# Kernel optimization log

Measured on AMD Instinct MI355X. Metric: run time of the kernel, lower is better.

Reference implementation:

```python
import jax, jax.numpy as jnp
import numpy as np

B, S, D_MODEL, D_ATT = 4, 4096, 512, 64
EPS = 1e-5


def setup_inputs() -> dict:
    key = jax.random.key(0)
    ks = jax.random.split(key, 10)
    s_in = 1.0 / np.sqrt(D_MODEL)
    return {
        "x": jax.random.normal(ks[0], (B, S, D_MODEL), jnp.float32),
        "Wq": jax.random.uniform(ks[1], (D_MODEL, D_ATT), jnp.float32, -s_in, s_in),
        "bq": jax.random.uniform(ks[2], (D_ATT,), jnp.float32, -s_in, s_in),
        "Wk": jax.random.uniform(ks[3], (D_MODEL, D_ATT), jnp.float32, -s_in, s_in),
        "bk": jax.random.uniform(ks[4], (D_ATT,), jnp.float32, -s_in, s_in),
        "Wv": jax.random.uniform(ks[5], (D_MODEL, D_MODEL), jnp.float32, -s_in, s_in),
        "bv": jax.random.uniform(ks[6], (D_MODEL,), jnp.float32, -s_in, s_in),
        "gamma": jnp.ones((D_MODEL,), jnp.float32),
        "beta": jnp.zeros((D_MODEL,), jnp.float32),
    }


def reference(x, Wq, bq, Wk, bk, Wv, bv, gamma, beta):
    # Linear projections (torch Linear: x @ W^T + b; here W stored as [in, out])
    q = jnp.einsum("bsd,de->bse", x, Wq) + bq          # [B,S,d_att]
    k = jnp.einsum("bsd,de->bse", x, Wk) + bk          # [B,S,d_att]
    v = jnp.einsum("bsd,de->bse", x, Wv) + bv          # [B,S,d_model]
    # NOTE: original has NO 1/sqrt(d) scaling -- faithful to source.
    scores = jnp.einsum("bqe,bke->bqk", q, k)          # [B,S,S]
    seq = x.shape[1]
    causal = jnp.tril(jnp.ones((seq, seq), dtype=bool))
    scores = jnp.where(causal, scores, -jnp.inf)
    attn = jax.nn.softmax(scores, axis=-1)
    o = jnp.einsum("bqk,bkd->bqd", attn, v)            # [B,S,d_model]
    # residual + LayerNorm over last dim
    y = x + o
    mu = jnp.mean(y, axis=-1, keepdims=True)
    var = jnp.mean(jnp.square(y - mu), axis=-1, keepdims=True)
    return (y - mu) * jax.lax.rsqrt(var + EPS) * gamma + beta
```

## Files before the change

kernel.cpp:

```cpp
#include <hip/hip_runtime.h>

#define NB 4
#define SEQ 4096
#define DM 512
#define DA 64
#define LOG2E 1.44269504f

typedef __attribute__((ext_vector_type(8))) short bf16x8;
typedef __attribute__((ext_vector_type(4))) float f32x4;
typedef __attribute__((ext_vector_type(16))) float f32x16;
typedef __attribute__((address_space(3))) unsigned int lds_u32;
typedef const __attribute__((address_space(1))) unsigned int glb_u32;

__device__ __forceinline__ unsigned short f2bf(float f) {
  unsigned u = __float_as_uint(f);
  u += 0x7fffu + ((u >> 16) & 1u);
  return (unsigned short)(u >> 16);
}

__device__ __forceinline__ float bf2f(unsigned short h) {
  return __uint_as_float(((unsigned)h) << 16);
}

__device__ __forceinline__ unsigned cvt_pk_bf16(float lo, float hi) {
  unsigned r;
  asm("v_cvt_pk_bf16_f32 %0, %1, %2" : "=v"(r) : "v"(lo), "v"(hi));
  return r;
}

__device__ __forceinline__ float fexp2(float x) {
  float r;
  asm("v_exp_f32 %0, %1" : "=v"(r) : "v"(x));
  return r;
}

__device__ __forceinline__ void g2lds16(const unsigned short* g, unsigned short* l) {
  __builtin_amdgcn_global_load_lds((glb_u32*)g, (lds_u32*)l, 16, 0, 0);
}

__global__ void cast_x_kernel(const float* __restrict__ x, unsigned short* __restrict__ xb) {
  size_t i = ((size_t)blockIdx.x * blockDim.x + threadIdx.x) * 4;
  float4 v = *(const float4*)(x + i);
  ushort4 o;
  o.x = f2bf(v.x); o.y = f2bf(v.y); o.z = f2bf(v.z); o.w = f2bf(v.w);
  *(ushort4*)(xb + i) = o;
}

__global__ void prep_w_kernel(const float* __restrict__ Wq, const float* __restrict__ bq,
                              const float* __restrict__ Wk, const float* __restrict__ bk,
                              const float* __restrict__ Wv, const float* __restrict__ bv,
                              unsigned short* __restrict__ Wt, float* __restrict__ bias) {
  int n = blockIdx.x;
  for (int k = threadIdx.x; k < DM; k += blockDim.x) {
    float w;
    if (n < 64)       w = Wq[(size_t)k * DA + n];
    else if (n < 128) w = Wk[(size_t)k * DA + (n - 64)];
    else              w = Wv[(size_t)k * DM + (n - 128)];
    Wt[(size_t)n * DM + k] = f2bf(w);
  }
  if (threadIdx.x == 0)
    bias[n] = (n < 64) ? bq[n] : (n < 128) ? bk[n - 64] : bv[n - 128];
}

__launch_bounds__(256)
__global__ void proj_kernel(const unsigned short* __restrict__ xb,
                            const unsigned short* __restrict__ Wt,
                            const float* __restrict__ bias,
                            unsigned short* __restrict__ qws,
                            unsigned short* __restrict__ kp,
                            unsigned short* __restrict__ vp) {
  int C0 = blockIdx.x * 128;
  int R0 = blockIdx.y * 128;
  int tid = threadIdx.x;
  int w = tid >> 6, lane = tid & 63;
  int g = (lane >> 4) & 3, c15 = lane & 15;
  int wr = w >> 1, wc = w & 1;

  __shared__ unsigned short Ab[2][8192];
  __shared__ unsigned short Bb[2][8192];

  int row0 = tid >> 3;
  int scol = (tid & 7) ^ (row0 & 7);
  const unsigned short* srcA = xb + (size_t)(R0 + row0) * DM + scol * 8;
  const unsigned short* srcB = Wt + (size_t)(C0 + row0) * DM + scol * 8;

  auto stage = [&](int t, int kk) {
    for (int r = 0; r < 4; r++)
      g2lds16(srcA + (size_t)(r * 32) * DM + kk, &Ab[t][(r * 32 + w * 8) * 64]);
    for (int r = 0; r < 4; r++)
      g2lds16(srcB + (size_t)(r * 32) * DM + kk, &Bb[t][(r * 32 + w * 8) * 64]);
  };

  f32x4 acc[4][4];
#pragma unroll
  for (int i = 0; i < 4; i++)
#pragma unroll
    for (int j = 0; j < 4; j++) acc[i][j] = (f32x4)0.0f;

  stage(0, 0);
  __syncthreads();
  int t = 0;
  for (int s = 0; s < 8; s++) {
    if (s < 7) stage(t ^ 1, (s + 1) * 64);
    const unsigned short* A = &Ab[t][0];
    const unsigned short* B = &Bb[t][0];
#pragma unroll
    for (int kc = 0; kc < 2; kc++) {
      bf16x8 a[4], bb2[4];
#pragma unroll
      for (int i = 0; i < 4; i++) {
        int row = wr * 64 + i * 16 + c15;
        a[i] = *(const bf16x8*)&A[row * 64 + (((kc << 2) | g) ^ (row & 7)) * 8];
      }
#pragma unroll
      for (int j = 0; j < 4; j++) {
        int row = wc * 64 + j * 16 + c15;
        bb2[j] = *(const bf16x8*)&B[row * 64 + (((kc << 2) | g) ^ (row & 7)) * 8];
      }
#pragma unroll
      for (int i = 0; i < 4; i++)
#pragma unroll
        for (int j = 0; j < 4; j++)
          acc[i][j] = __builtin_amdgcn_mfma_f32_16x16x32_bf16(a[i], bb2[j], acc[i][j], 0, 0, 0);
    }
    __syncthreads();
    t ^= 1;
  }

  unsigned short* tw = (w < 2) ? (&Ab[0][0] + w * 4608) : (&Bb[0][0] + (w - 2) * 4608);
  int n0 = C0 + wc * 64;
#pragma unroll
  for (int j = 0; j < 4; j++) {
    int ncol = n0 + j * 16 + c15;
    float bv_ = bias[ncol];
    float qs = (ncol < 64) ? LOG2E : 1.0f;
#pragma unroll
    for (int i = 0; i < 4; i++)
#pragma unroll
      for (int r = 0; r < 4; r++) {
        int sl = i * 16 + g * 4 + r;
        tw[sl * 72 + j * 16 + c15] = f2bf((acc[i][j][r] + bv_) * qs);
      }
  }

  int RR = R0 + wr * 64;
  int b = RR >> 12, ktc = (RR & (SEQ - 1)) >> 6;
  if (n0 == 0) {
    for (int it = 0; it < 8; it++) {
      int rid = it * 64 + lane;
      int sl = rid >> 3, grp = rid & 7;
      bf16x8 vd = *(const bf16x8*)&tw[sl * 72 + grp * 8];
      *(bf16x8*)(qws + (size_t)(RR + sl) * DA + grp * 8) = vd;
    }
  } else if (n0 == 64) {
    for (int slot = 0; slot < 8; slot++) {
      bf16x8 vd = *(const bf16x8*)&tw[lane * 72 + slot * 8];
      *(bf16x8*)(kp + ((((size_t)b * 64 + ktc) * 8 + slot) * 64 + lane) * 8) = vd;
    }
  } else {
    int dvbase = n0 - 128;
    int dv = dvbase + lane;
    int dvc2 = dv >> 7, dvrow = dv & 127;
    for (int slot = 0; slot < 8; slot++) {
      union { unsigned short u[8]; bf16x8 h8; } pk;
#pragma unroll
      for (int j = 0; j < 8; j++) {
        int key = ((slot >> 2) << 5) | (((slot >> 1) & 1) << 4) | ((j >> 2) << 3) |
                  ((slot & 1) << 2) | (j & 3);
        pk.u[j] = tw[key * 72 + lane];
      }
      *(bf16x8*)(vp + (((((size_t)(b * 4 + dvc2)) * 64 + ktc) * 8 + slot) * 128 + dvrow) * 8) = pk.h8;
    }
  }
}

__launch_bounds__(256, 3)
__global__ void attn_kernel(const unsigned short* __restrict__ qws,
                            const unsigned short* __restrict__ kp,
                            const unsigned short* __restrict__ vp,
                            unsigned short* __restrict__ ob16) {
  int x = blockIdx.x, b = x >> 2, dvc = x & 3;
  int strip = 127 - blockIdx.y;
  int qrow32 = strip * 32;
  int n = (strip >> 1) + 1;
  int tid = threadIdx.x, w = tid >> 6, lane = tid & 63;
  int l31 = lane & 31, lh = lane >> 5;

  __shared__ unsigned short abuf[4][32][138];
  __shared__ float lbuf[4][32], Lfin[32];

  size_t bS = (size_t)b * SEQ;

  bf16x8 qf[4];
#pragma unroll
  for (int c = 0; c < 4; c++)
    qf[c] = *(const bf16x8*)(qws + (bS + qrow32 + l31) * DA + c * 16 + lh * 8);

  const unsigned short* kbase = kp + (size_t)b * 64 * 4096 + lh * 512 + l31 * 8;
  const unsigned short* vbase = vp + (size_t)(b * 4 + dvc) * 64 * 8192 + lh * 1024 + l31 * 8;

  f32x16 acc[4];
#pragma unroll
  for (int dt = 0; dt < 4; dt++) acc[dt] = (f32x16)0.0f;
  float la0 = 0.0f, la1 = 0.0f, la2 = 0.0f, la3 = 0.0f;

  for (int t = w; t < n; t += 4) {
    const unsigned short* kt_ = kbase + (size_t)t * 4096;
    const unsigned short* vt_ = vbase + (size_t)t * 8192;

    bf16x8 kf[4][2];
#pragma unroll
    for (int c = 0; c < 4; c++)
#pragma unroll
      for (int s2 = 0; s2 < 2; s2++)
        kf[c][s2] = *(const bf16x8*)(kt_ + c * 1024 + s2 * 256);
    bf16x8 vbA[4];
#pragma unroll
    for (int dt = 0; dt < 4; dt++)
      vbA[dt] = *(const bf16x8*)(vt_ + dt * 256);

    f32x16 sc[2];
    sc[0] = (f32x16)0.0f; sc[1] = (f32x16)0.0f;
    __builtin_amdgcn_s_setprio(1);
#pragma unroll
    for (int c = 0; c < 4; c++)
#pragma unroll
      for (int s2 = 0; s2 < 2; s2++)
        sc[s2] = __builtin_amdgcn_mfma_f32_32x32x16_bf16(kf[c][s2], qf[c], sc[s2], 0, 0, 0);
    __builtin_amdgcn_s_setprio(0);

    if (t == n - 1) {
      int kt = t * 64, qrow = qrow32 + l31;
#pragma unroll
      for (int s2 = 0; s2 < 2; s2++)
#pragma unroll
        for (int p = 0; p < 16; p++) {
          int key = kt + s2 * 32 + (p & 3) + 8 * (p >> 2) + 4 * lh;
          if (key > qrow) sc[s2][p] = -1e30f;
        }
    }

#pragma unroll
    for (int s2 = 0; s2 < 2; s2++)
#pragma unroll
      for (int p = 0; p < 16; p += 4) {
        float p0 = fexp2(sc[s2][p + 0]);
        float p1 = fexp2(sc[s2][p + 1]);
        float p2 = fexp2(sc[s2][p + 2]);
        float p3 = fexp2(sc[s2][p + 3]);
        sc[s2][p + 0] = p0; sc[s2][p + 1] = p1;
        sc[s2][p + 2] = p2; sc[s2][p + 3] = p3;
        la0 += p0; la1 += p1; la2 += p2; la3 += p3;
      }

    bf16x8 pa[4];
#pragma unroll
    for (int c = 0; c < 4; c++) {
      union { unsigned u[4]; bf16x8 h; } pu;
      int s2 = c >> 1, o = (c & 1) * 8;
      pu.u[0] = cvt_pk_bf16(sc[s2][o + 0], sc[s2][o + 1]);
      pu.u[1] = cvt_pk_bf16(sc[s2][o + 2], sc[s2][o + 3]);
      pu.u[2] = cvt_pk_bf16(sc[s2][o + 4], sc[s2][o + 5]);
      pu.u[3] = cvt_pk_bf16(sc[s2][o + 6], sc[s2][o + 7]);
      pa[c] = pu.h;
    }

    __builtin_amdgcn_s_setprio(1);
#pragma unroll
    for (int c = 0; c < 4; c++) {
      bf16x8 vbB[4];
      if (c < 3) {
#pragma unroll
        for (int dt = 0; dt < 4; dt++)
          vbB[dt] = *(const bf16x8*)(vt_ + (c + 1) * 2048 + dt * 256);
      }
#pragma unroll
      for (int dt = 0; dt < 4; dt++)
        acc[dt] = __builtin_amdgcn_mfma_f32_32x32x16_bf16(vbA[dt], pa[c], acc[dt], 0, 0, 0);
      if (c < 3) {
#pragma unroll
        for (int dt = 0; dt < 4; dt++) vbA[dt] = vbB[dt];
      }
    }
    __builtin_amdgcn_s_setprio(0);
  }

  float l_run = (la0 + la1) + (la2 + la3);
  l_run += __shfl_xor(l_run, 32);
  if (lh == 0) lbuf[w][l31] = l_run;
  __syncthreads();
  if (w == 0 && lh == 0)
    Lfin[l31] = lbuf[0][l31] + lbuf[1][l31] + lbuf[2][l31] + lbuf[3][l31];
#pragma unroll
  for (int dt = 0; dt < 4; dt++)
#pragma unroll
    for (int p = 0; p < 16; p += 2) {
      int dv = dt * 32 + (p & 3) + 8 * (p >> 2) + 4 * lh;
      *(unsigned*)&abuf[w][l31][dv] = cvt_pk_bf16(acc[dt][p], acc[dt][p + 1]);
    }
  __syncthreads();

  int q = w * 8 + (l31 >> 2);
  int ch = (l31 & 3) * 32 + lh * 16;
  float s[16];
#pragma unroll
  for (int k = 0; k < 16; k++) s[k] = 0.0f;
#pragma unroll
  for (int v = 0; v < 4; v++) {
    bf16x8 a0 = *(const bf16x8*)&abuf[v][q][ch];
    bf16x8 a1 = *(const bf16x8*)&abuf[v][q][ch + 8];
#pragma unroll
    for (int k = 0; k < 8; k++) {
      s[k] += bf2f((unsigned short)a0[k]);
      s[8 + k] += bf2f((unsigned short)a1[k]);
    }
  }
  float inv = 1.0f / Lfin[q];
  union { unsigned u[8]; bf16x8 h[2]; } o;
#pragma unroll
  for (int k = 0; k < 8; k++)
    o.u[k] = cvt_pk_bf16(s[2 * k] * inv, s[2 * k + 1] * inv);
  unsigned short* dst = ob16 + (bS + qrow32 + q) * DM + dvc * 128 + ch;
  *(bf16x8*)dst = o.h[0];
  *(bf16x8*)(dst + 8) = o.h[1];
}

__launch_bounds__(256)
__global__ void ln_kernel(const float* __restrict__ x, const unsigned short* __restrict__ o,
                          const float* __restrict__ gamma, const float* __restrict__ beta,
                          float* __restrict__ out) {
  int wid = threadIdx.x >> 6, lane = threadIdx.x & 63;
  size_t row = (size_t)blockIdx.x * 4 + wid;
  size_t base = row * DM + lane * 8;
  float4 xa = *(const float4*)(x + base);
  float4 xb2 = *(const float4*)(x + base + 4);
  bf16x8 ov = *(const bf16x8*)(o + base);
  float y[8] = {xa.x + bf2f((unsigned short)ov[0]), xa.y + bf2f((unsigned short)ov[1]),
                xa.z + bf2f((unsigned short)ov[2]), xa.w + bf2f((unsigned short)ov[3]),
                xb2.x + bf2f((unsigned short)ov[4]), xb2.y + bf2f((unsigned short)ov[5]),
                xb2.z + bf2f((unsigned short)ov[6]), xb2.w + bf2f((unsigned short)ov[7])};
  float s1 = 0.0f, s2 = 0.0f;
  for (int j = 0; j < 8; j++) { s1 += y[j]; s2 += y[j] * y[j]; }
  for (int m = 1; m < 64; m <<= 1) { s1 += __shfl_xor(s1, m); s2 += __shfl_xor(s2, m); }
  float mu = s1 * (1.0f / DM);
  float var = s2 * (1.0f / DM) - mu * mu;
  float rs = rsqrtf(var + 1e-5f);
  int c = lane * 8;
  for (int j = 0; j < 8; j++)
    out[base + j] = (y[j] - mu) * rs * gamma[c + j] + beta[c + j];
}

extern "C" void kernel_launch(void* const* d_in, const int* in_sizes, int n_in,
                              void* d_out, int out_size, void* d_ws, size_t ws_size,
                              hipStream_t stream) {
  const float* x     = (const float*)d_in[0];
  const float* Wq    = (const float*)d_in[1];
  const float* bq    = (const float*)d_in[2];
  const float* Wk    = (const float*)d_in[3];
  const float* bk    = (const float*)d_in[4];
  const float* Wv    = (const float*)d_in[5];
  const float* bv    = (const float*)d_in[6];
  const float* gamma = (const float*)d_in[7];
  const float* beta  = (const float*)d_in[8];
  float* out = (float*)d_out;

  char* ws = (char*)d_ws;
  unsigned short* xb   = (unsigned short*)(ws + 0);
  unsigned short* ob16 = (unsigned short*)(ws + 0);
  unsigned short* qws  = (unsigned short*)(ws + 16777216);
  unsigned short* kp   = (unsigned short*)(ws + 18874368);
  unsigned short* vp   = (unsigned short*)(ws + 20971520);
  unsigned short* Wt   = (unsigned short*)(ws + 37748736);
  float*          bias = (float*)(ws + 38404096);

  cast_x_kernel<<<8192, 256, 0, stream>>>(x, xb);
  prep_w_kernel<<<640, 256, 0, stream>>>(Wq, bq, Wk, bk, Wv, bv, Wt, bias);
  proj_kernel<<<dim3(5, 128), 256, 0, stream>>>(xb, Wt, bias, qws, kp, vp);
  attn_kernel<<<dim3(16, 128), 256, 0, stream>>>(qws, kp, vp, ob16);
  ln_kernel<<<4096, 256, 0, stream>>>(x, ob16, gamma, beta, out);
}
```

Measured before the change: 135.3 us.

## Process 64 query rows per attention block to reuse K/V tiles

Each attention block now handles two 32-row query strips (64 rows), so every loaded K and V fragment feeds two MFMAs instead of one. This halves global K/V traffic per query and halves the grid height. In exchange, register use roughly doubles (two accumulator sets), launch bounds drop to one block per SIMD group, and the V double-buffer prefetch is removed. The epilogue is run twice through shared memory with extra barriers.

```diff
diff --git a/kernel.cpp b/kernel.cpp
--- a/kernel.cpp
+++ b/kernel.cpp
@@ -174,35 +174,38 @@
   }
 }
 
-__launch_bounds__(256, 3)
+__launch_bounds__(256, 1)
 __global__ void attn_kernel(const unsigned short* __restrict__ qws,
                             const unsigned short* __restrict__ kp,
                             const unsigned short* __restrict__ vp,
                             unsigned short* __restrict__ ob16) {
   int x = blockIdx.x, b = x >> 2, dvc = x & 3;
-  int strip = 127 - blockIdx.y;
-  int qrow32 = strip * 32;
-  int n = (strip >> 1) + 1;
+  int strip = 63 - blockIdx.y;
+  int qrow64 = strip * 64;
+  int n = strip + 1;
   int tid = threadIdx.x, w = tid >> 6, lane = tid & 63;
   int l31 = lane & 31, lh = lane >> 5;
 
   __shared__ unsigned short abuf[4][32][138];
-  __shared__ float lbuf[4][32], Lfin[32];
+  __shared__ float lbuf[4][2][32];
 
   size_t bS = (size_t)b * SEQ;
 
-  bf16x8 qf[4];
-#pragma unroll
-  for (int c = 0; c < 4; c++)
-    qf[c] = *(const bf16x8*)(qws + (bS + qrow32 + l31) * DA + c * 16 + lh * 8);
+  bf16x8 qf0[4], qf1[4];
+#pragma unroll
+  for (int c = 0; c < 4; c++) {
+    qf0[c] = *(const bf16x8*)(qws + (bS + qrow64 + l31) * DA + c * 16 + lh * 8);
+    qf1[c] = *(const bf16x8*)(qws + (bS + qrow64 + 32 + l31) * DA + c * 16 + lh * 8);
+  }
 
   const unsigned short* kbase = kp + (size_t)b * 64 * 4096 + lh * 512 + l31 * 8;
   const unsigned short* vbase = vp + (size_t)(b * 4 + dvc) * 64 * 8192 + lh * 1024 + l31 * 8;
 
-  f32x16 acc[4];
-#pragma unroll
-  for (int dt = 0; dt < 4; dt++) acc[dt] = (f32x16)0.0f;
+  f32x16 acc0[4], acc1[4];
+#pragma unroll
+  for (int dt = 0; dt < 4; dt++) { acc0[dt] = (f32x16)0.0f; acc1[dt] = (f32x16)0.0f; }
   float la0 = 0.0f, la1 = 0.0f, la2 = 0.0f, la3 = 0.0f;
+  float lb0 = 0.0f, lb1 = 0.0f, lb2 = 0.0f, lb3 = 0.0f;
 
   for (int t = w; t < n; t += 4) {
     const unsigned short* kt_ = kbase + (size_t)t * 4096;
@@ -214,29 +217,30 @@
 #pragma unroll
       for (int s2 = 0; s2 < 2; s2++)
         kf[c][s2] = *(const bf16x8*)(kt_ + c * 1024 + s2 * 256);
-    bf16x8 vbA[4];
-#pragma unroll
-    for (int dt = 0; dt < 4; dt++)
-      vbA[dt] = *(const bf16x8*)(vt_ + dt * 256);
-
-    f32x16 sc[2];
-    sc[0] = (f32x16)0.0f; sc[1] = (f32x16)0.0f;
+
+    f32x16 sc0[2], sc1[2];
+    sc0[0] = (f32x16)0.0f; sc0[1] = (f32x16)0.0f;
+    sc1[0] = (f32x16)0.0f; sc1[1] = (f32x16)0.0f;
     __builtin_amdgcn_s_setprio(1);
 #pragma unroll
     for (int c = 0; c < 4; c++)
 #pragma unroll
-      for (int s2 = 0; s2 < 2; s2++)
-        sc[s2] = __builtin_amdgcn_mfma_f32_32x32x16_bf16(kf[c][s2], qf[c], sc[s2], 0, 0, 0);
+      for (int s2 = 0; s2 < 2; s2++) {
+        sc0[s2] = __builtin_amdgcn_mfma_f32_32x32x16_bf16(kf[c][s2], qf0[c], sc0[s2], 0, 0, 0);
+        sc1[s2] = __builtin_amdgcn_mfma_f32_32x32x16_bf16(kf[c][s2], qf1[c], sc1[s2], 0, 0, 0);
+      }
     __builtin_amdgcn_s_setprio(0);
 
     if (t == n - 1) {
-      int kt = t * 64, qrow = qrow32 + l31;
+      int kt = t * 64;
+      int qr0 = qrow64 + l31, qr1 = qrow64 + 32 + l31;
 #pragma unroll
       for (int s2 = 0; s2 < 2; s2++)
 #pragma unroll
         for (int p = 0; p < 16; p++) {
           int key = kt + s2 * 32 + (p & 3) + 8 * (p >> 2) + 4 * lh;
-          if (key > qrow) sc[s2][p] = -1e30f;
+          if (key > qr0) sc0[s2][p] = -1e30f;
+          if (key > qr1) sc1[s2][p] = -1e30f;
         }
     }
 
@@ -244,85 +248,130 @@
     for (int s2 = 0; s2 < 2; s2++)
 #pragma unroll
       for (int p = 0; p < 16; p += 4) {
-        float p0 = fexp2(sc[s2][p + 0]);
-        float p1 = fexp2(sc[s2][p + 1]);
-        float p2 = fexp2(sc[s2][p + 2]);
-        float p3 = fexp2(sc[s2][p + 3]);
-        sc[s2][p + 0] = p0; sc[s2][p + 1] = p1;
-        sc[s2][p + 2] = p2; sc[s2][p + 3] = p3;
+        float p0 = fexp2(sc0[s2][p + 0]);
+        float p1 = fexp2(sc0[s2][p + 1]);
+        float p2 = fexp2(sc0[s2][p + 2]);
+        float p3 = fexp2(sc0[s2][p + 3]);
+        sc0[s2][p + 0] = p0; sc0[s2][p + 1] = p1;
+        sc0[s2][p + 2] = p2; sc0[s2][p + 3] = p3;
         la0 += p0; la1 += p1; la2 += p2; la3 += p3;
-      }
-
-    bf16x8 pa[4];
+        float q0 = fexp2(sc1[s2][p + 0]);
+        float q1 = fexp2(sc1[s2][p + 1]);
+        float q2 = fexp2(sc1[s2][p + 2]);
+        float q3 = fexp2(sc1[s2][p + 3]);
+        sc1[s2][p + 0] = q0; sc1[s2][p + 1] = q1;
+        sc1[s2][p + 2] = q2; sc1[s2][p + 3] = q3;
+        lb0 += q0; lb1 += q1; lb2 += q2; lb3 += q3;
+      }
+
+    bf16x8 pa0[4], pa1[4];
 #pragma unroll
     for (int c = 0; c < 4; c++) {
       union { unsigned u[4]; bf16x8 h; } pu;
       int s2 = c >> 1, o = (c & 1) * 8;
-      pu.u[0] = cvt_pk_bf16(sc[s2][o + 0], sc[s2][o + 1]);
-      pu.u[1] = cvt_pk_bf16(sc[s2][o + 2], sc[s2][o + 3]);
-      pu.u[2] = cvt_pk_bf16(sc[s2][o + 4], sc[s2][o + 5]);
-      pu.u[3] = cvt_pk_bf16(sc[s2][o + 6], sc[s2][o + 7]);
-      pa[c] = pu.h;
+      pu.u[0] = cvt_pk_bf16(sc0[s2][o + 0], sc0[s2][o + 1]);
+      pu.u[1] = cvt_pk_bf16(sc0[s2][o + 2], sc0[s2][o + 3]);
+      pu.u[2] = cvt_pk_bf16(sc0[s2][o + 4], sc0[s2][o + 5]);
+      pu.u[3] = cvt_pk_bf16(sc0[s2][o + 6], sc0[s2][o + 7]);
+      pa0[c] = pu.h;
+      pu.u[0] = cvt_pk_bf16(sc1[s2][o + 0], sc1[s2][o + 1]);
+      pu.u[1] = cvt_pk_bf16(sc1[s2][o + 2], sc1[s2][o + 3]);
+      pu.u[2] = cvt_pk_bf16(sc1[s2][o + 4], sc1[s2][o + 5]);
+      pu.u[3] = cvt_pk_bf16(sc1[s2][o + 6], sc1[s2][o + 7]);
+      pa1[c] = pu.h;
     }
 
     __builtin_amdgcn_s_setprio(1);
 #pragma unroll
     for (int c = 0; c < 4; c++) {
-      bf16x8 vbB[4];
-      if (c < 3) {
-#pragma unroll
-        for (int dt = 0; dt < 4; dt++)
-          vbB[dt] = *(const bf16x8*)(vt_ + (c + 1) * 2048 + dt * 256);
-      }
+      bf16x8 vb[4];
 #pragma unroll
       for (int dt = 0; dt < 4; dt++)
-        acc[dt] = __builtin_amdgcn_mfma_f32_32x32x16_bf16(vbA[dt], pa[c], acc[dt], 0, 0, 0);
-      if (c < 3) {
-#pragma unroll
-        for (int dt = 0; dt < 4; dt++) vbA[dt] = vbB[dt];
+        vb[dt] = *(const bf16x8*)(vt_ + c * 2048 + dt * 256);
+#pragma unroll
+      for (int dt = 0; dt < 4; dt++) {
+        acc0[dt] = __builtin_amdgcn_mfma_f32_32x32x16_bf16(vb[dt], pa0[c], acc0[dt], 0, 0, 0);
+        acc1[dt] = __builtin_amdgcn_mfma_f32_32x32x16_bf16(vb[dt], pa1[c], acc1[dt], 0, 0, 0);
       }
     }
     __builtin_amdgcn_s_setprio(0);
   }
 
-  float l_run = (la0 + la1) + (la2 + la3);
-  l_run += __shfl_xor(l_run, 32);
-  if (lh == 0) lbuf[w][l31] = l_run;
-  __syncthreads();
-  if (w == 0 && lh == 0)
-    Lfin[l31] = lbuf[0][l31] + lbuf[1][l31] + lbuf[2][l31] + lbuf[3][l31];
+  float l0 = (la0 + la1) + (la2 + la3);
+  l0 += __shfl_xor(l0, 32);
+  float l1 = (lb0 + lb1) + (lb2 + lb3);
+  l1 += __shfl_xor(l1, 32);
+  if (lh == 0) { lbuf[w][0][l31] = l0; lbuf[w][1][l31] = l1; }
+
+  int q = w * 8 + (l31 >> 2);
+  int ch = (l31 & 3) * 32 + lh * 16;
+
 #pragma unroll
   for (int dt = 0; dt < 4; dt++)
 #pragma unroll
     for (int p = 0; p < 16; p += 2) {
       int dv = dt * 32 + (p & 3) + 8 * (p >> 2) + 4 * lh;
-      *(unsigned*)&abuf[w][l31][dv] = cvt_pk_bf16(acc[dt][p], acc[dt][p + 1]);
+      *(unsigned*)&abuf[w][l31][dv] = cvt_pk_bf16(acc0[dt][p], acc0[dt][p + 1]);
     }
   __syncthreads();
-
-  int q = w * 8 + (l31 >> 2);
-  int ch = (l31 & 3) * 32 + lh * 16;
-  float s[16];
-#pragma unroll
-  for (int k = 0; k < 16; k++) s[k] = 0.0f;
-#pragma unroll
-  for (int v = 0; v < 4; v++) {
-    bf16x8 a0 = *(const bf16x8*)&abuf[v][q][ch];
-    bf16x8 a1 = *(const bf16x8*)&abuf[v][q][ch + 8];
-#pragma unroll
-    for (int k = 0; k < 8; k++) {
-      s[k] += bf2f((unsigned short)a0[k]);
-      s[8 + k] += bf2f((unsigned short)a1[k]);
-    }
-  }
-  float inv = 1.0f / Lfin[q];
-  union { unsigned u[8]; bf16x8 h[2]; } o;
-#pragma unroll
-  for (int k = 0; k < 8; k++)
-    o.u[k] = cvt_pk_bf16(s[2 * k] * inv, s[2 * k + 1] * inv);
-  unsigned short* dst = ob16 + (bS + qrow32 + q) * DM + dvc * 128 + ch;
-  *(bf16x8*)dst = o.h[0];
-  *(bf16x8*)(dst + 8) = o.h[1];
+  {
+    float L = lbuf[0][0][q] + lbuf[1][0][q] + lbuf[2][0][q] + lbuf[3][0][q];
+    float s[16];
+#pragma unroll
+    for (int k = 0; k < 16; k++) s[k] = 0.0f;
+#pragma unroll
+    for (int v = 0; v < 4; v++) {
+      bf16x8 a0 = *(const bf16x8*)&abuf[v][q][ch];
+      bf16x8 a1 = *(const bf16x8*)&abuf[v][q][ch + 8];
+#pragma unroll
+      for (int k = 0; k < 8; k++) {
+        s[k] += bf2f((unsigned short)a0[k]);
+        s[8 + k] += bf2f((unsigned short)a1[k]);
+      }
+    }
+    float inv = 1.0f / L;
+    union { unsigned u[8]; bf16x8 h[2]; } o;
+#pragma unroll
+    for (int k = 0; k < 8; k++)
+      o.u[k] = cvt_pk_bf16(s[2 * k] * inv, s[2 * k + 1] * inv);
+    unsigned short* dst = ob16 + (bS + qrow64 + q) * DM + dvc * 128 + ch;
+    *(bf16x8*)dst = o.h[0];
+    *(bf16x8*)(dst + 8) = o.h[1];
+  }
+  __syncthreads();
+
+#pragma unroll
+  for (int dt = 0; dt < 4; dt++)
+#pragma unroll
+    for (int p = 0; p < 16; p += 2) {
+      int dv = dt * 32 + (p & 3) + 8 * (p >> 2) + 4 * lh;
+      *(unsigned*)&abuf[w][l31][dv] = cvt_pk_bf16(acc1[dt][p], acc1[dt][p + 1]);
+    }
+  __syncthreads();
+  {
+    float L = lbuf[0][1][q] + lbuf[1][1][q] + lbuf[2][1][q] + lbuf[3][1][q];
+    float s[16];
+#pragma unroll
+    for (int k = 0; k < 16; k++) s[k] = 0.0f;
+#pragma unroll
+    for (int v = 0; v < 4; v++) {
+      bf16x8 a0 = *(const bf16x8*)&abuf[v][q][ch];
+      bf16x8 a1 = *(const bf16x8*)&abuf[v][q][ch + 8];
+#pragma unroll
+      for (int k = 0; k < 8; k++) {
+        s[k] += bf2f((unsigned short)a0[k]);
+        s[8 + k] += bf2f((unsigned short)a1[k]);
+      }
+    }
+    float inv = 1.0f / L;
+    union { unsigned u[8]; bf16x8 h[2]; } o;
+#pragma unroll
+    for (int k = 0; k < 8; k++)
+      o.u[k] = cvt_pk_bf16(s[2 * k] * inv, s[2 * k + 1] * inv);
+    unsigned short* dst = ob16 + (bS + qrow64 + 32 + q) * DM + dvc * 128 + ch;
+    *(bf16x8*)dst = o.h[0];
+    *(bf16x8*)(dst + 8) = o.h[1];
+  }
 }
 
 __launch_bounds__(256)
@@ -376,6 +425,6 @@
   cast_x_kernel<<<8192, 256, 0, stream>>>(x, xb);
   prep_w_kernel<<<640, 256, 0, stream>>>(Wq, bq, Wk, bk, Wv, bv, Wt, bias);
   proj_kernel<<<dim3(5, 128), 256, 0, stream>>>(xb, Wt, bias, qws, kp, vp);
-  attn_kernel<<<dim3(16, 128), 256, 0, stream>>>(qws, kp, vp, ob16);
+  attn_kernel<<<dim3(16, 64), 256, 0, stream>>>(qws, kp, vp, ob16);
   ln_kernel<<<4096, 256, 0, stream>>>(x, ob16, gamma, beta, out);
 }
```

New measurement: 181.5 us. +34.2%, slower.
